# Optimization experiments

Hardware: AMD Instinct MI355X
Metric: run time of the kernel (lower is better)

The kernel has to match this reference:

```python
import jax, jax.numpy as jnp
import numpy as np

N = 262144  # points per batch (~4096 rays x 64 samples)
FDIM = 64   # plane feature dim
S = 512     # base plane resolution


def setup_inputs() -> dict:
    key = jax.random.key(0)
    ks = jax.random.split(key, 10)
    x = jax.random.uniform(ks[0], (N, 3), dtype=jnp.float32, minval=-1.0, maxval=1.0)
    rays_o = jnp.array([[0.0, 0.0, 1.5]], dtype=jnp.float32)  # ray origin; distances straddle 1.5/2.0
    scale = jnp.ones((3,), dtype=jnp.float32)
    plane = lambda k, s: jax.random.normal(k, (FDIM, s, s), dtype=jnp.float32)
    return {
        'x': x, 'rays_o': rays_o, 'scale': scale,
        'xy_plane': plane(ks[1], S), 'yz_plane': plane(ks[2], S), 'xz_plane': plane(ks[3], S),
        'xy_plane1': plane(ks[4], S // 2), 'yz_plane1': plane(ks[5], S // 2), 'xz_plane1': plane(ks[6], S // 2),
        'xy_plane2': plane(ks[7], S // 4), 'yz_plane2': plane(ks[8], S // 4), 'xz_plane2': plane(ks[9], S // 4),
    }


def bilinear_sample(plane, coords):
    """F.grid_sample(mode='bilinear', align_corners=True, padding_mode='zeros').
    plane: [C, H, W]; coords: [N, 2] with (x, y) in [-1, 1] (x indexes W).
    Returns [N, C]."""
    C, H, W = plane.shape
    fx = (coords[:, 0] + 1.0) * 0.5 * (W - 1)
    fy = (coords[:, 1] + 1.0) * 0.5 * (H - 1)
    x0 = jnp.floor(fx)
    y0 = jnp.floor(fy)
    wx = fx - x0
    wy = fy - y0
    x0i = x0.astype(jnp.int32)
    y0i = y0.astype(jnp.int32)

    def gather(xi, yi):
        valid = (xi >= 0) & (xi < W) & (yi >= 0) & (yi < H)
        xc = jnp.clip(xi, 0, W - 1)
        yc = jnp.clip(yi, 0, H - 1)
        v = plane[:, yc, xc]  # [C, N]
        return jnp.where(valid[None, :], v, 0.0)

    v00 = gather(x0i, y0i)
    v01 = gather(x0i + 1, y0i)
    v10 = gather(x0i, y0i + 1)
    v11 = gather(x0i + 1, y0i + 1)
    out = (v00 * (1 - wx) * (1 - wy) + v01 * wx * (1 - wy)
           + v10 * (1 - wx) * wy + v11 * wx * wy)  # [C, N]
    return out.T


def forward(x, rays_o, scale, xy0, yz0, xz0, xy1, yz1, xz1, xy2, yz2, xz2):
    xs = x * scale[None, :]
    xy_c = xs[:, :2]                                   # (x, y)
    xz_c = jnp.stack([xs[:, 0], xs[:, 2]], axis=-1)    # (x, z)
    yz_c = xs[:, 1:]                                   # (y, z)

    # laplace breakpoints: first index with distance > 1.5 / > 2.0 from rays_o[0]
    d = jnp.linalg.norm(rays_o[0][None, :] - xs, axis=-1)
    c1 = d > 1.5
    c2 = d > 2.0
    break1 = jnp.where(c1.any(), jnp.argmax(c1), 0)
    break2 = jnp.where(c2.any(), jnp.argmax(c2), 0)
    idx = jnp.arange(x.shape[0])
    # level 0: [0, break1), level 1: [break1, break2), level 2: [break2, N)
    level = jnp.where(idx < break1, 0, jnp.where(idx < break2, 1, 2))[:, None]

    def tri(p0, p1, p2, c):
        s0 = bilinear_sample(p0, c)
        s1 = bilinear_sample(p1, c)
        s2 = bilinear_sample(p2, c)
        # laplace: level1 = fine + half, level2 = fine + half + quarter
        return jnp.where(level == 0, s0, jnp.where(level == 1, s0 + s1, s0 + s1 + s2))

    return (tri(xy0, xy1, xy2, xy_c)
            + tri(xz0, xz1, xz2, xz_c)
            + tri(yz0, yz1, yz2, yz_c))


def reference(x, rays_o, scale, xy_plane, yz_plane, xz_plane, xy_plane1, yz_plane1, xz_plane1, xy_plane2, yz_plane2, xz_plane2):
    return forward(x, rays_o, scale, xy_plane, yz_plane, xz_plane,
                   xy_plane1, yz_plane1, xz_plane1,
                   xy_plane2, yz_plane2, xz_plane2)
```

## Files before the change

kernel.cpp:

```cpp
#include <hip/hip_runtime.h>
#include <hip/hip_fp16.h>

#define NPTS 262144
#define FDIM 64
#define NCELL 32768

typedef float vfloat4 __attribute__((ext_vector_type(4)));

__global__ __launch_bounds__(256) void break_kernel(const float* __restrict__ x,
                                                    const float* __restrict__ rays_o,
                                                    const float* __restrict__ scale,
                                                    unsigned* __restrict__ breaks) {
  const unsigned t = blockIdx.x * 256u + threadIdx.x;
  const float r0 = rays_o[0], r1 = rays_o[1], r2 = rays_o[2];
  const float s0 = scale[0], s1 = scale[1], s2 = scale[2];
  unsigned b1 = 0xFFFFFFFFu, b2 = 0xFFFFFFFFu;
  for (unsigned p = t; p < NPTS; p += 65536u) {
    const float dx = r0 - x[p * 3 + 0] * s0;
    const float dy = r1 - x[p * 3 + 1] * s1;
    const float dz = r2 - x[p * 3 + 2] * s2;
    const float d = sqrtf(__fadd_rn(__fadd_rn(__fmul_rn(dx, dx), __fmul_rn(dy, dy)),
                                    __fmul_rn(dz, dz)));
    if (d > 1.5f) b1 = min(b1, p);
    if (d > 2.0f) b2 = min(b2, p);
  }
#pragma unroll
  for (int o = 32; o > 0; o >>= 1) {
    b1 = min(b1, (unsigned)__shfl_down((int)b1, o, 64));
    b2 = min(b2, (unsigned)__shfl_down((int)b2, o, 64));
  }
  if ((threadIdx.x & 63) == 0) {
    atomicMin(&breaks[0], b1);
    atomicMin(&breaks[1], b2);
  }
}

__device__ __forceinline__ unsigned part5(unsigned v) {
  v &= 31u;
  v = (v | (v << 8)) & 0x100Fu;
  v = (v | (v << 4)) & 0x10C3u;
  v = (v | (v << 2)) & 0x1249u;
  return v;
}

__device__ __forceinline__ unsigned cell_key(float x0, float x1, float x2) {
  const int cx = min(max((int)((x0 + 1.0f) * 16.0f), 0), 31);
  const int cy = min(max((int)((x1 + 1.0f) * 16.0f), 0), 31);
  const int cz = min(max((int)((x2 + 1.0f) * 16.0f), 0), 31);
  return part5((unsigned)cx) | (part5((unsigned)cy) << 1) | (part5((unsigned)cz) << 2);
}

__global__ __launch_bounds__(256) void breakhist_kernel(const float* __restrict__ x,
                                                        const float* __restrict__ rays_o,
                                                        const float* __restrict__ scale,
                                                        unsigned* __restrict__ breaks,
                                                        unsigned* __restrict__ hist) {
  const unsigned t = blockIdx.x * 256u + threadIdx.x;
  const float s0 = scale[0], s1 = scale[1], s2 = scale[2];
  const float xs0 = x[t * 3 + 0] * s0;
  const float xs1 = x[t * 3 + 1] * s1;
  const float xs2 = x[t * 3 + 2] * s2;
  const float dx = rays_o[0] - xs0;
  const float dy = rays_o[1] - xs1;
  const float dz = rays_o[2] - xs2;
  const float d = sqrtf(__fadd_rn(__fadd_rn(__fmul_rn(dx, dx), __fmul_rn(dy, dy)),
                                  __fmul_rn(dz, dz)));
  unsigned b1 = (d > 1.5f) ? t : 0xFFFFFFFFu;
  unsigned b2 = (d > 2.0f) ? t : 0xFFFFFFFFu;
#pragma unroll
  for (int o = 32; o > 0; o >>= 1) {
    b1 = min(b1, (unsigned)__shfl_down((int)b1, o, 64));
    b2 = min(b2, (unsigned)__shfl_down((int)b2, o, 64));
  }
  if ((threadIdx.x & 63) == 0) {
    atomicMin(&breaks[0], b1);
    atomicMin(&breaks[1], b2);
  }
  const unsigned key = cell_key(xs0, xs1, xs2);
  atomicAdd(&hist[key], 1u);
}

__global__ __launch_bounds__(256) void scan1_kernel(unsigned* __restrict__ hist,
                                                    unsigned* __restrict__ partials) {
  const int cell = blockIdx.x * 256 + threadIdx.x;
  const int tid = threadIdx.x;
  const unsigned h = hist[cell];
  __shared__ unsigned ls[256];
  ls[tid] = h;
  __syncthreads();
  for (int d = 1; d < 256; d <<= 1) {
    const unsigned add = (tid >= d) ? ls[tid - d] : 0u;
    __syncthreads();
    ls[tid] += add;
    __syncthreads();
  }
  hist[cell] = ls[tid] - h;
  if (tid == 255) partials[blockIdx.x] = ls[255];
}

__global__ __launch_bounds__(128) void scan2_kernel(unsigned* __restrict__ partials) {
  const int tid = threadIdx.x;
  const unsigned h = partials[tid];
  __shared__ unsigned ls[128];
  ls[tid] = h;
  __syncthreads();
  for (int d = 1; d < 128; d <<= 1) {
    const unsigned add = (tid >= d) ? ls[tid - d] : 0u;
    __syncthreads();
    ls[tid] += add;
    __syncthreads();
  }
  partials[tid] = ls[tid] - h;
}

__global__ __launch_bounds__(256) void scatter_kernel(const float* __restrict__ x,
                                                      const float* __restrict__ scale,
                                                      const unsigned* __restrict__ breaks,
                                                      unsigned* __restrict__ offs,
                                                      const unsigned* __restrict__ partials,
                                                      float4* __restrict__ xs_sorted) {
  const unsigned t = blockIdx.x * 256u + threadIdx.x;
  const float s0 = scale[0], s1 = scale[1], s2 = scale[2];
  const float xs0 = x[t * 3 + 0] * s0;
  const float xs1 = x[t * 3 + 1] * s1;
  const float xs2 = x[t * 3 + 2] * s2;
  const unsigned key = cell_key(xs0, xs1, xs2);
  const unsigned pos = atomicAdd(&offs[key], 1u) + partials[key >> 8];
  unsigned b1 = breaks[0]; if (b1 >= NPTS) b1 = 0;
  unsigned b2 = breaks[1]; if (b2 >= NPTS) b2 = 0;
  const unsigned lvl = (t < b1) ? 0u : ((t < b2) ? 1u : 2u);
  float4 v;
  v.x = xs0; v.y = xs1; v.z = xs2;
  v.w = __uint_as_float(t | (lvl << 18));
  xs_sorted[pos] = v;
}

#define TPIX 128

struct TransposeArgs {
  const float* src[9];
  __half* dst[9];
  int tile_hi[9];
  int SS[9];
};

union H8 { uint4 u; __half h[8]; };

__global__ __launch_bounds__(256) void transpose_all(TransposeArgs a) {
  const int tile = blockIdx.x;
  int pi = 0;
#pragma unroll
  for (int i = 0; i < 9; ++i) {
    if (tile >= a.tile_hi[i]) pi = i + 1;
  }
  const int lo = (pi == 0) ? 0 : a.tile_hi[pi - 1];
  const float* __restrict__ src = a.src[pi];
  __half* __restrict__ dst = a.dst[pi];
  const size_t SS = (size_t)a.SS[pi];

  const int t = threadIdx.x;
  const int slot = t >> 3;
  const int c8 = t & 7;
  const size_t p0 = (size_t)(tile - lo) * TPIX + (size_t)slot * 4;
  const float* __restrict__ srcb = src + (size_t)(c8 * 8) * SS + p0;

  H8 h[4];
#pragma unroll
  for (int k = 0; k < 8; ++k) {
    const float4 v = *(const float4*)(srcb + (size_t)k * SS);
    h[0].h[k] = __float2half(v.x);
    h[1].h[k] = __float2half(v.y);
    h[2].h[k] = __float2half(v.z);
    h[3].h[k] = __float2half(v.w);
  }
#pragma unroll
  for (int r = 0; r < 4; ++r) {
    *(uint4*)(dst + (p0 + (size_t)r) * FDIM + c8 * 8) = h[r].u;
  }
}

__device__ __forceinline__ void bilinear_weights(int W, float cx, float cy,
                                                 float& w00, float& w01, float& w10, float& w11,
                                                 int& xc0, int& xc1, int& yc0, int& yc1) {
  const float Wm1 = (float)(W - 1);
  const float fx = (cx + 1.0f) * 0.5f * Wm1;
  const float fy = (cy + 1.0f) * 0.5f * Wm1;
  const float x0f = floorf(fx), y0f = floorf(fy);
  const float wx = fx - x0f, wy = fy - y0f;
  const int ix = (int)x0f, iy = (int)y0f;
  const int ix1 = ix + 1, iy1 = iy + 1;
  const bool vx0 = (ix >= 0) && (ix < W);
  const bool vx1 = (ix1 >= 0) && (ix1 < W);
  const bool vy0 = (iy >= 0) && (iy < W);
  const bool vy1 = (iy1 >= 0) && (iy1 < W);
  xc0 = min(max(ix, 0), W - 1);
  xc1 = min(max(ix1, 0), W - 1);
  yc0 = min(max(iy, 0), W - 1);
  yc1 = min(max(iy1, 0), W - 1);
  w00 = (1.0f - wx) * (1.0f - wy) * (float)(vx0 && vy0);
  w01 = wx * (1.0f - wy) * (float)(vx1 && vy0);
  w10 = (1.0f - wx) * wy * (float)(vx0 && vy1);
  w11 = wx * wy * (float)(vx1 && vy1);
}

__device__ __forceinline__ void sample8_t(const __half* __restrict__ pl, int W,
                                          float cx, float cy, int j8, float acc[8]) {
  float w00, w01, w10, w11;
  int xc0, xc1, yc0, yc1;
  bilinear_weights(W, cx, cy, w00, w01, w10, w11, xc0, xc1, yc0, yc1);
  const __half* b00 = pl + ((size_t)(yc0 * W + xc0) * FDIM + j8);
  const __half* b01 = pl + ((size_t)(yc0 * W + xc1) * FDIM + j8);
  const __half* b10 = pl + ((size_t)(yc1 * W + xc0) * FDIM + j8);
  const __half* b11 = pl + ((size_t)(yc1 * W + xc1) * FDIM + j8);
  H8 v00, v01, v10, v11;
  v00.u = *(const uint4*)b00;
  v01.u = *(const uint4*)b01;
  v10.u = *(const uint4*)b10;
  v11.u = *(const uint4*)b11;
#pragma unroll
  for (int k = 0; k < 8; ++k) {
    acc[k] += w00 * __half2float(v00.h[k]) + w01 * __half2float(v01.h[k]) +
              w10 * __half2float(v10.h[k]) + w11 * __half2float(v11.h[k]);
  }
}

__device__ __forceinline__ void sample8_d(const float* __restrict__ pl, int W,
                                          float cx, float cy, int j8, float acc[8]) {
  float w00, w01, w10, w11;
  int xc0, xc1, yc0, yc1;
  bilinear_weights(W, cx, cy, w00, w01, w10, w11, xc0, xc1, yc0, yc1);
  const size_t SS = (size_t)W * W;
  const int i00 = yc0 * W + xc0, i01 = yc0 * W + xc1;
  const int i10 = yc1 * W + xc0, i11 = yc1 * W + xc1;
#pragma unroll
  for (int k = 0; k < 8; ++k) {
    const size_t co = (size_t)(j8 + k) * SS;
    acc[k] += w00 * pl[co + i00] + w01 * pl[co + i01] +
              w10 * pl[co + i10] + w11 * pl[co + i11];
  }
}

struct PlanesH { const __half* p[9]; };
struct PlanesF { const float* p[9]; };

#define SAMPLE_BLOCKS (NPTS * 8 / 256)
#define XCD_CHUNK (SAMPLE_BLOCKS / 8)

__global__ __launch_bounds__(256) void sample_kernel(const float4* __restrict__ xs_sorted,
                                                     PlanesH tp, float* __restrict__ out) {
  const unsigned b = blockIdx.x;
  const unsigned sb = (b & 7u) * XCD_CHUNK + (b >> 3);
  const int t = (int)(sb * 256u + threadIdx.x);
  const int slot = t >> 3;
  const int j8 = (t & 7) * 8;
  const float4 ps = xs_sorted[slot];
  const unsigned w = __float_as_uint(ps.w);
  const int p = (int)(w & 0x3FFFFu);
  const int level = (int)(w >> 18);
  float acc[8];
#pragma unroll
  for (int k = 0; k < 8; ++k) acc[k] = 0.0f;
  sample8_t(tp.p[0], 512, ps.x, ps.y, j8, acc);
  sample8_t(tp.p[1], 512, ps.y, ps.z, j8, acc);
  sample8_t(tp.p[2], 512, ps.x, ps.z, j8, acc);
  if (level >= 1) {
    sample8_t(tp.p[3], 256, ps.x, ps.y, j8, acc);
    sample8_t(tp.p[4], 256, ps.y, ps.z, j8, acc);
    sample8_t(tp.p[5], 256, ps.x, ps.z, j8, acc);
  }
  if (level >= 2) {
    sample8_t(tp.p[6], 128, ps.x, ps.y, j8, acc);
    sample8_t(tp.p[7], 128, ps.y, ps.z, j8, acc);
    sample8_t(tp.p[8], 128, ps.x, ps.z, j8, acc);
  }
  float* o = out + (size_t)p * FDIM + j8;
  vfloat4 lo = {acc[0], acc[1], acc[2], acc[3]};
  vfloat4 hi = {acc[4], acc[5], acc[6], acc[7]};
  __builtin_nontemporal_store(lo, (vfloat4*)o);
  __builtin_nontemporal_store(hi, (vfloat4*)(o + 4));
}

__global__ __launch_bounds__(256) void sample_kernel_direct(const float* __restrict__ x,
                                                            const float* __restrict__ scale,
                                                            const unsigned* __restrict__ breaks,
                                                            PlanesF tp, float* __restrict__ out) {
  const int t = blockIdx.x * 256 + threadIdx.x;
  const int p = t >> 3;
  const int j8 = (t & 7) * 8;
  const float s0 = scale[0], s1 = scale[1], s2 = scale[2];
  const float xs0 = x[p * 3 + 0] * s0;
  const float xs1 = x[p * 3 + 1] * s1;
  const float xs2 = x[p * 3 + 2] * s2;
  unsigned b1 = breaks[0]; if (b1 >= NPTS) b1 = 0;
  unsigned b2 = breaks[1]; if (b2 >= NPTS) b2 = 0;
  const unsigned pu = (unsigned)p;
  const int level = (pu < b1) ? 0 : ((pu < b2) ? 1 : 2);
  float acc[8];
#pragma unroll
  for (int k = 0; k < 8; ++k) acc[k] = 0.0f;
  sample8_d(tp.p[0], 512, xs0, xs1, j8, acc);
  sample8_d(tp.p[1], 512, xs1, xs2, j8, acc);
  sample8_d(tp.p[2], 512, xs0, xs2, j8, acc);
  if (level >= 1) {
    sample8_d(tp.p[3], 256, xs0, xs1, j8, acc);
    sample8_d(tp.p[4], 256, xs1, xs2, j8, acc);
    sample8_d(tp.p[5], 256, xs0, xs2, j8, acc);
  }
  if (level >= 2) {
    sample8_d(tp.p[6], 128, xs0, xs1, j8, acc);
    sample8_d(tp.p[7], 128, xs1, xs2, j8, acc);
    sample8_d(tp.p[8], 128, xs0, xs2, j8, acc);
  }
  float4* o4 = (float4*)(out + (size_t)p * FDIM + j8);
  o4[0] = make_float4(acc[0], acc[1], acc[2], acc[3]);
  o4[1] = make_float4(acc[4], acc[5], acc[6], acc[7]);
}

extern "C" void kernel_launch(void* const* d_in, const int* in_sizes, int n_in,
                              void* d_out, int out_size, void* d_ws, size_t ws_size,
                              hipStream_t stream) {
  const float* x = (const float*)d_in[0];
  const float* rays_o = (const float*)d_in[1];
  const float* scale = (const float*)d_in[2];
  const float* pl32[9];
  for (int i = 0; i < 9; ++i) pl32[i] = (const float*)d_in[3 + i];
  float* out = (float*)d_out;

  unsigned char* ws = (unsigned char*)d_ws;
  unsigned* breaks = (unsigned*)ws;
  unsigned* partials = (unsigned*)(ws + 128);
  unsigned* hist = (unsigned*)(ws + 1024);
  float4* xs_sorted = (float4*)(ws + 1024 + NCELL * 4);
  const size_t planes_off = 1024 + (size_t)NCELL * 4 + (size_t)NPTS * 16;

  (void)hipMemsetAsync(d_ws, 0xFF, 8, stream);

  const int Ss[3] = {512, 256, 128};
  size_t need = planes_off;
  for (int l = 0; l < 3; ++l) need += 3 * (size_t)Ss[l] * Ss[l] * FDIM * sizeof(__half);

  if (ws_size >= need) {
    (void)hipMemsetAsync(hist, 0, NCELL * 4, stream);
    breakhist_kernel<<<NPTS / 256, 256, 0, stream>>>(x, rays_o, scale, breaks, hist);
    scan1_kernel<<<NCELL / 256, 256, 0, stream>>>(hist, partials);
    scan2_kernel<<<1, 128, 0, stream>>>(partials);
    scatter_kernel<<<NPTS / 256, 256, 0, stream>>>(x, scale, breaks, hist, partials, xs_sorted);

    PlanesH tp;
    TransposeArgs ta;
    size_t off = planes_off;
    int tiles_acc = 0;
    for (int l = 0; l < 3; ++l) {
      const int S = Ss[l];
      const int SS = S * S;
      for (int o = 0; o < 3; ++o) {
        const int i = l * 3 + o;
        __half* dst = (__half*)(ws + off);
        tp.p[i] = dst;
        ta.src[i] = pl32[i];
        ta.dst[i] = dst;
        ta.SS[i] = SS;
        tiles_acc += SS / TPIX;
        ta.tile_hi[i] = tiles_acc;
        off += (size_t)SS * FDIM * sizeof(__half);
      }
    }
    transpose_all<<<tiles_acc, 256, 0, stream>>>(ta);
    sample_kernel<<<SAMPLE_BLOCKS, 256, 0, stream>>>(xs_sorted, tp, out);
  } else {
    break_kernel<<<256, 256, 0, stream>>>(x, rays_o, scale, breaks);
    PlanesF tf;
    for (int i = 0; i < 9; ++i) tf.p[i] = pl32[i];
    sample_kernel_direct<<<(NPTS * 8) / 256, 256, 0, stream>>>(x, scale, breaks, tf, out);
  }
}
```

Baseline: 490.4 us.

## Coarsen spatial sort grid to 16^3 cells with single-block scan and permuted transpose tiles

Reduces the Morton-sorted cell grid from 32^3 to 16^3, so the prefix scan fits in one 1024-thread block and one kernel launch plus the partials array go away. The transpose kernel also visits tiles in a permuted order (multiplying by 997 modulo the tile count), apparently to spread memory traffic across channels. Coarser cells mean more atomic contention per cell in the histogram and scatter, and weaker spatial locality for the later gather kernel.

Result: no change. 486.7 us (-0.7%).

```diff
diff --git a/kernel.cpp b/kernel.cpp
--- a/kernel.cpp
+++ b/kernel.cpp
@@ -3,7 +3,7 @@
 
 #define NPTS 262144
 #define FDIM 64
-#define NCELL 32768
+#define NCELL 4096
 
 typedef float vfloat4 __attribute__((ext_vector_type(4)));
 
@@ -35,19 +35,18 @@
   }
 }
 
-__device__ __forceinline__ unsigned part5(unsigned v) {
-  v &= 31u;
-  v = (v | (v << 8)) & 0x100Fu;
-  v = (v | (v << 4)) & 0x10C3u;
-  v = (v | (v << 2)) & 0x1249u;
+__device__ __forceinline__ unsigned part4(unsigned v) {
+  v &= 15u;
+  v = (v | (v << 4)) & 0x0C3u;
+  v = (v | (v << 2)) & 0x249u;
   return v;
 }
 
 __device__ __forceinline__ unsigned cell_key(float x0, float x1, float x2) {
-  const int cx = min(max((int)((x0 + 1.0f) * 16.0f), 0), 31);
-  const int cy = min(max((int)((x1 + 1.0f) * 16.0f), 0), 31);
-  const int cz = min(max((int)((x2 + 1.0f) * 16.0f), 0), 31);
-  return part5((unsigned)cx) | (part5((unsigned)cy) << 1) | (part5((unsigned)cz) << 2);
+  const int cx = min(max((int)((x0 + 1.0f) * 8.0f), 0), 15);
+  const int cy = min(max((int)((x1 + 1.0f) * 8.0f), 0), 15);
+  const int cz = min(max((int)((x2 + 1.0f) * 8.0f), 0), 15);
+  return part4((unsigned)cx) | (part4((unsigned)cy) << 1) | (part4((unsigned)cz) << 2);
 }
 
 __global__ __launch_bounds__(256) void breakhist_kernel(const float* __restrict__ x,
@@ -80,44 +79,35 @@
   atomicAdd(&hist[key], 1u);
 }
 
-__global__ __launch_bounds__(256) void scan1_kernel(unsigned* __restrict__ hist,
-                                                    unsigned* __restrict__ partials) {
-  const int cell = blockIdx.x * 256 + threadIdx.x;
+__global__ __launch_bounds__(1024) void scan_kernel(unsigned* __restrict__ hist) {
   const int tid = threadIdx.x;
-  const unsigned h = hist[cell];
-  __shared__ unsigned ls[256];
-  ls[tid] = h;
+  uint4 h = ((uint4*)hist)[tid];
+  const unsigned i0 = h.x;
+  const unsigned i1 = i0 + h.y;
+  const unsigned i2 = i1 + h.z;
+  const unsigned i3 = i2 + h.w;
+  __shared__ unsigned ls[1024];
+  ls[tid] = i3;
   __syncthreads();
-  for (int d = 1; d < 256; d <<= 1) {
+  for (int d = 1; d < 1024; d <<= 1) {
     const unsigned add = (tid >= d) ? ls[tid - d] : 0u;
     __syncthreads();
     ls[tid] += add;
     __syncthreads();
   }
-  hist[cell] = ls[tid] - h;
-  if (tid == 255) partials[blockIdx.x] = ls[255];
-}
-
-__global__ __launch_bounds__(128) void scan2_kernel(unsigned* __restrict__ partials) {
-  const int tid = threadIdx.x;
-  const unsigned h = partials[tid];
-  __shared__ unsigned ls[128];
-  ls[tid] = h;
-  __syncthreads();
-  for (int d = 1; d < 128; d <<= 1) {
-    const unsigned add = (tid >= d) ? ls[tid - d] : 0u;
-    __syncthreads();
-    ls[tid] += add;
-    __syncthreads();
-  }
-  partials[tid] = ls[tid] - h;
+  const unsigned base = ls[tid] - i3;
+  uint4 o;
+  o.x = base;
+  o.y = base + i0;
+  o.z = base + i1;
+  o.w = base + i2;
+  ((uint4*)hist)[tid] = o;
 }
 
 __global__ __launch_bounds__(256) void scatter_kernel(const float* __restrict__ x,
                                                       const float* __restrict__ scale,
                                                       const unsigned* __restrict__ breaks,
                                                       unsigned* __restrict__ offs,
-                                                      const unsigned* __restrict__ partials,
                                                       float4* __restrict__ xs_sorted) {
   const unsigned t = blockIdx.x * 256u + threadIdx.x;
   const float s0 = scale[0], s1 = scale[1], s2 = scale[2];
@@ -125,7 +115,7 @@
   const float xs1 = x[t * 3 + 1] * s1;
   const float xs2 = x[t * 3 + 2] * s2;
   const unsigned key = cell_key(xs0, xs1, xs2);
-  const unsigned pos = atomicAdd(&offs[key], 1u) + partials[key >> 8];
+  const unsigned pos = atomicAdd(&offs[key], 1u);
   unsigned b1 = breaks[0]; if (b1 >= NPTS) b1 = 0;
   unsigned b2 = breaks[1]; if (b2 >= NPTS) b2 = 0;
   const unsigned lvl = (t < b1) ? 0u : ((t < b2) ? 1u : 2u);
@@ -158,10 +148,13 @@
   __half* __restrict__ dst = a.dst[pi];
   const size_t SS = (size_t)a.SS[pi];
 
+  const int ntm = (int)(SS / TPIX) - 1;
+  const int tl = ((tile - lo) * 997) & ntm;
+
   const int t = threadIdx.x;
   const int slot = t >> 3;
   const int c8 = t & 7;
-  const size_t p0 = (size_t)(tile - lo) * TPIX + (size_t)slot * 4;
+  const size_t p0 = (size_t)tl * TPIX + (size_t)slot * 4;
   const float* __restrict__ srcb = src + (size_t)(c8 * 8) * SS + p0;
 
   H8 h[4];
@@ -328,7 +321,6 @@
 
   unsigned char* ws = (unsigned char*)d_ws;
   unsigned* breaks = (unsigned*)ws;
-  unsigned* partials = (unsigned*)(ws + 128);
   unsigned* hist = (unsigned*)(ws + 1024);
   float4* xs_sorted = (float4*)(ws + 1024 + NCELL * 4);
   const size_t planes_off = 1024 + (size_t)NCELL * 4 + (size_t)NPTS * 16;
@@ -342,9 +334,8 @@
   if (ws_size >= need) {
     (void)hipMemsetAsync(hist, 0, NCELL * 4, stream);
     breakhist_kernel<<<NPTS / 256, 256, 0, stream>>>(x, rays_o, scale, breaks, hist);
-    scan1_kernel<<<NCELL / 256, 256, 0, stream>>>(hist, partials);
-    scan2_kernel<<<1, 128, 0, stream>>>(partials);
-    scatter_kernel<<<NPTS / 256, 256, 0, stream>>>(x, scale, breaks, hist, partials, xs_sorted);
+    scan_kernel<<<1, 1024, 0, stream>>>(hist);
+    scatter_kernel<<<NPTS / 256, 256, 0, stream>>>(x, scale, breaks, hist, xs_sorted);
 
     PlanesH tp;
     TransposeArgs ta;
```
